# Kernel optimization log

Measured on AMD Instinct MI355X. Metric: run time of the kernel, lower is better.

The kernel has to match this reference:

```python
import jax, jax.numpy as jnp
import numpy as np

IGNORE_INDEX = -100
LABEL_SMOOTHING = 0.0


def setup_inputs() -> dict:
    key = jax.random.key(0)
    k1, k2, k3, k4 = jax.random.split(key, 4)
    BT, H, V = 4096, 1024, 32000
    x = jax.random.normal(k1, (BT, H), dtype=jnp.float32)
    target = jax.random.randint(k2, (BT,), 0, V, dtype=jnp.int64)
    # scale weight so logits have O(1) std (realistic trained lm_head scale)
    weight = jax.random.normal(k3, (V, H), dtype=jnp.float32) * 0.02
    bias = jax.random.normal(k4, (V,), dtype=jnp.float32) * 0.02
    return {"x": x, "target": target, "weight": weight, "bias": bias}


def reference(x, target, weight, bias):
    # x: [BT, H], weight: [V, H], bias: [V], target: [BT]
    V = weight.shape[0]
    ls = LABEL_SMOOTHING
    logits = x @ weight.T + bias                     # [BT, V]
    lse = jax.nn.logsumexp(logits, axis=-1)          # [BT]
    # gather logit at the target class (clip so ignore_index rows stay in-bounds)
    safe_t = jnp.clip(target, 0, V - 1)
    x_y = jnp.take_along_axis(logits, safe_t[:, None], axis=-1)[:, 0]
    # CE with label smoothing: (1-ls)*(lse - x_y) + ls*lse - (ls/V)*sum_j x_j
    per_row = (1.0 - ls) * (lse - x_y)
    if ls > 0.0:
        per_row = per_row + ls * lse - (ls / V) * jnp.sum(logits, axis=-1)
    valid = target != IGNORE_INDEX
    per_row = jnp.where(valid, per_row, 0.0)
    n_non_ignore = jnp.sum(valid).astype(per_row.dtype)
    loss = jnp.sum(per_row) / n_non_ignore
    return loss
```

## Files before the change

kernel.cpp:

```cpp
#include <hip/hip_runtime.h>
#include <hip/hip_bf16.h>
#include <stdint.h>


typedef float f16v __attribute__((ext_vector_type(16)));
typedef int v8i __attribute__((ext_vector_type(8)));
typedef int v4i __attribute__((ext_vector_type(4)));

__device__ __forceinline__ unsigned pk_fp8(float4 v) {
  int w = 0;
  w = __builtin_amdgcn_cvt_pk_fp8_f32(v.x, v.y, w, false);
  w = __builtin_amdgcn_cvt_pk_fp8_f32(v.z, v.w, w, true);
  return (unsigned)w;
}

__global__ __launch_bounds__(256) void cast_stage_k(const float* __restrict__ inW,
                                                    char* __restrict__ outW,
                                                    const float* __restrict__ inX,
                                                    char* __restrict__ outX,
                                                    int sW, int sTot) {
  __shared__ unsigned lds[8192];
  int s = blockIdx.x;
  const float* in;
  char* out;
  if (s < sW) { in = inW; out = outW; }
  else        { in = inX; out = outX; s -= sW; }
  const int t = threadIdx.x;
  const float4* src = (const float4*)in + (long)s * 8192 + t;
  const int u0 = ((t >> 3) << 8) + (t & 7);
#pragma unroll 4
  for (int r = 0; r < 32; ++r) lds[u0 + r * 8] = pk_fp8(src[r * 256]);
  __syncthreads();
  const uint4* lv = (const uint4*)lds;
  uint4* dst = (uint4*)(out + (long)s * 32768);
#pragma unroll
  for (int p = 0; p < 8; ++p) dst[p * 256 + t] = lv[p * 256 + t];
}

__device__ __forceinline__ v8i ldfrag(const char* p) {
  const v4i* q = (const v4i*)p;
  v4i lo = q[0];
  v4i hi = q[1];
  return __builtin_shufflevector(lo, hi, 0, 1, 2, 3, 4, 5, 6, 7);
}

#define MFMA1(A, B, C) \
  __builtin_amdgcn_mfma_scale_f32_32x32x64_f8f6f4(A, B, C, 0, 0, 0, 127, 0, 127)

__global__ __launch_bounds__(256, 4)
void gemm_sumexp(const char* __restrict__ Xf, const char* __restrict__ Wf,
                 const float* __restrict__ bias, float* __restrict__ partials,
                 int H, int BT) {
  __shared__ float rowsum[2][128];

  const int tid = threadIdx.x;
  const int w = tid >> 6, lane = tid & 63;
  const int wr = w >> 1, wc = w & 1;
  const int l32 = lane & 31, kh = lane >> 5;

  const int by = blockIdx.x;
  const int bx = blockIdx.y;
  const int m0 = bx * 128, n0 = by * 128;

  const int Rb = bx * 4 + wr * 2;
  const int Nb = by * 4 + wc * 2;

  const char* pA0 = Xf + (long)(Rb + 0) * 32768 + lane * 32;
  const char* pA1 = Xf + (long)(Rb + 1) * 32768 + lane * 32;
  const char* pB0 = Wf + (long)(Nb + 0) * 32768 + lane * 32;
  const char* pB1 = Wf + (long)(Nb + 1) * 32768 + lane * 32;

  f16v acc[2][2];
#pragma unroll
  for (int mi = 0; mi < 2; mi++)
#pragma unroll
    for (int ni = 0; ni < 2; ni++)
#pragma unroll
      for (int r = 0; r < 16; r++) acc[mi][ni][r] = 0.f;

  const int nG = H >> 6;
#pragma unroll 4
  for (int g = 0; g < nG; g++) {
    v8i a0 = ldfrag(pA0); pA0 += 2048;
    v8i a1 = ldfrag(pA1); pA1 += 2048;
    v8i b0 = ldfrag(pB0); pB0 += 2048;
    v8i b1 = ldfrag(pB1); pB1 += 2048;
    acc[0][0] = MFMA1(a0, b0, acc[0][0]);
    acc[0][1] = MFMA1(a0, b1, acc[0][1]);
    acc[1][0] = MFMA1(a1, b0, acc[1][0]);
    acc[1][1] = MFMA1(a1, b1, acc[1][1]);
  }

  float bv[2];
  bv[0] = bias[n0 + wc * 64 + l32];
  bv[1] = bias[n0 + wc * 64 + 32 + l32];

#pragma unroll
  for (int mi = 0; mi < 2; mi++) {
    float p[16];
#pragma unroll
    for (int r = 0; r < 16; r++) p[r] = 0.f;
#pragma unroll
    for (int ni = 0; ni < 2; ni++)
#pragma unroll
      for (int r = 0; r < 16; r++) p[r] += __expf(acc[mi][ni][r] + bv[ni]);
#pragma unroll
    for (int off = 1; off < 32; off <<= 1)
#pragma unroll
      for (int r = 0; r < 16; r++) p[r] += __shfl_xor(p[r], off, 32);
    if (l32 == 0) {
#pragma unroll
      for (int r = 0; r < 16; r++)
        rowsum[wc][wr * 64 + mi * 32 + (r & 3) + 8 * (r >> 2) + 4 * kh] = p[r];
    }
  }
  __syncthreads();
  if (tid < 128)
    partials[(long)by * BT + m0 + tid] = rowsum[0][tid] + rowsum[1][tid];
}

__global__ __launch_bounds__(256)
void row_reduce(const float* __restrict__ partials, const float* __restrict__ x,
                const float* __restrict__ wt, const float* __restrict__ bias,
                const int* __restrict__ tgt, float* __restrict__ bsum,
                float* __restrict__ bcnt, int BT, int nCB, int H, int V) {
  const int w = threadIdx.x >> 6, lane = threadIdx.x & 63;
  const int row = blockIdx.x * 4 + w;
  float S = 0.f;
  for (int b = lane; b < nCB; b += 64) S += partials[(long)b * BT + row];
  const int t = tgt[row];
  const int st = min(max(t, 0), V - 1);
  const float4* xr = (const float4*)(x + (long)row * H);
  const float4* wr = (const float4*)(wt + (long)st * H);
  float d = 0.f;
  const int n4 = H >> 2;
  for (int i = lane; i < n4; i += 64) {
    float4 a = xr[i], b = wr[i];
    d += a.x * b.x + a.y * b.y + a.z * b.z + a.w * b.w;
  }
  for (int off = 32; off; off >>= 1) {
    S += __shfl_down(S, off, 64);
    d += __shfl_down(d, off, 64);
  }
  __shared__ float sp[4], sc[4];
  if (lane == 0) {
    bool valid = (t != -100);
    sp[w] = valid ? (logf(S) - (d + bias[st])) : 0.f;
    sc[w] = valid ? 1.f : 0.f;
  }
  __syncthreads();
  if (threadIdx.x == 0) {
    bsum[blockIdx.x] = sp[0] + sp[1] + sp[2] + sp[3];
    bcnt[blockIdx.x] = sc[0] + sc[1] + sc[2] + sc[3];
  }
}

__global__ void finalize(const float* __restrict__ bsum, const float* __restrict__ bcnt,
                         float* __restrict__ out, int nb) {
  float s = 0.f, c = 0.f;
  for (int i = threadIdx.x; i < nb; i += 64) { s += bsum[i]; c += bcnt[i]; }
  for (int off = 32; off; off >>= 1) {
    s += __shfl_down(s, off, 64);
    c += __shfl_down(c, off, 64);
  }
  if (threadIdx.x == 0) out[0] = s / c;
}

extern "C" void kernel_launch(void* const* d_in, const int* in_sizes, int n_in,
                              void* d_out, int out_size, void* d_ws, size_t ws_size,
                              hipStream_t stream) {
  const float* x = (const float*)d_in[0];
  const int* tgt = (const int*)d_in[1];
  const float* w = (const float*)d_in[2];
  const float* bias = (const float*)d_in[3];
  float* out = (float*)d_out;

  const int BT = in_sizes[1];
  const int V = in_sizes[3];
  const int H = in_sizes[0] / BT;
  const int nCB = V / 128;

  char* ws = (char*)d_ws;
  const long wb_bytes = (long)V * H;
  const long xb_bytes = (long)BT * H;
  char* Wf = ws;
  char* Xf = ws + wb_bytes;
  float* partials = (float*)(ws + wb_bytes + xb_bytes);
  float* bsum = partials + (long)nCB * BT;
  float* bcnt = bsum + (BT / 4);

  const int sW = V / 32;
  const int sTot = sW + BT / 32;
  cast_stage_k<<<sTot, 256, 0, stream>>>(w, Wf, x, Xf, sW, sTot);
  dim3 grid(nCB, BT / 128);
  gemm_sumexp<<<grid, 256, 0, stream>>>(Xf, Wf, bias, partials, H, BT);
  row_reduce<<<BT / 4, 256, 0, stream>>>(partials, x, w, bias, tgt, bsum, bcnt,
                                         BT, nCB, H, V);
  finalize<<<1, 64, 0, stream>>>(bsum, bcnt, out, BT / 4);
}
```

Baseline: 398.5 us.

## Keep weight tile resident in LDS and stream all input rows per block

Each block now owns 128 vocabulary columns. It loads that fp8 weight slab (128 KB) into LDS once with global_load_lds, then loops over every 256-row slab of the fp8 input, computing MFMA tiles and writing per-slab row sums of exp. The grid shrinks to one block per column tile with 512 threads. This is meant to roughly halve global/L2 traffic by reading weights once instead of once per row tile. The trade-off is that the large LDS footprint allows only one block per CU, which lowers occupancy and latency hiding for the streamed input loads.

```diff
diff --git a/kernel.cpp b/kernel.cpp
--- a/kernel.cpp
+++ b/kernel.cpp
@@ -47,76 +47,89 @@
 #define MFMA1(A, B, C) \
   __builtin_amdgcn_mfma_scale_f32_32x32x64_f8f6f4(A, B, C, 0, 0, 0, 127, 0, 127)
 
-__global__ __launch_bounds__(256, 4)
+__global__ __launch_bounds__(512, 2)
 void gemm_sumexp(const char* __restrict__ Xf, const char* __restrict__ Wf,
                  const float* __restrict__ bias, float* __restrict__ partials,
                  int H, int BT) {
-  __shared__ float rowsum[2][128];
+  __shared__ char wlds[131072];
+  __shared__ float rowsum[2][4][256];
 
   const int tid = threadIdx.x;
   const int w = tid >> 6, lane = tid & 63;
-  const int wr = w >> 1, wc = w & 1;
+  const int wr = w >> 2, wc = w & 3;
   const int l32 = lane & 31, kh = lane >> 5;
 
   const int by = blockIdx.x;
-  const int bx = blockIdx.y;
-  const int m0 = bx * 128, n0 = by * 128;
-
-  const int Rb = bx * 4 + wr * 2;
-  const int Nb = by * 4 + wc * 2;
-
-  const char* pA0 = Xf + (long)(Rb + 0) * 32768 + lane * 32;
-  const char* pA1 = Xf + (long)(Rb + 1) * 32768 + lane * 32;
-  const char* pB0 = Wf + (long)(Nb + 0) * 32768 + lane * 32;
-  const char* pB1 = Wf + (long)(Nb + 1) * 32768 + lane * 32;
-
-  f16v acc[2][2];
-#pragma unroll
-  for (int mi = 0; mi < 2; mi++)
-#pragma unroll
-    for (int ni = 0; ni < 2; ni++)
-#pragma unroll
-      for (int r = 0; r < 16; r++) acc[mi][ni][r] = 0.f;
-
+  const int n0 = by * 128;
+
+  {
+    const char* src = Wf + (long)by * 131072 + lane * 16;
+#pragma unroll
+    for (int r = 0; r < 16; ++r) {
+      const int i = w * 16 + r;
+      __builtin_amdgcn_global_load_lds(
+          (const __attribute__((address_space(1))) void*)(src + i * 1024),
+          (__attribute__((address_space(3))) void*)(wlds + i * 1024),
+          16, 0, 0);
+    }
+  }
+  __syncthreads();
+
+  const float bv = bias[n0 + wc * 32 + l32];
   const int nG = H >> 6;
+  const int nSlab = BT >> 8;
+
+  for (int s = 0; s < nSlab; ++s) {
+    f16v acc[4];
+#pragma unroll
+    for (int mi = 0; mi < 4; mi++)
+#pragma unroll
+      for (int r = 0; r < 16; r++) acc[mi][r] = 0.f;
+
+    const int Rb = s * 8 + wr * 4;
+    const char* pA0 = Xf + (long)(Rb + 0) * 32768 + lane * 32;
+    const char* pA1 = Xf + (long)(Rb + 1) * 32768 + lane * 32;
+    const char* pA2 = Xf + (long)(Rb + 2) * 32768 + lane * 32;
+    const char* pA3 = Xf + (long)(Rb + 3) * 32768 + lane * 32;
+    const char* pB = wlds + wc * 32768 + lane * 32;
+
 #pragma unroll 4
-  for (int g = 0; g < nG; g++) {
-    v8i a0 = ldfrag(pA0); pA0 += 2048;
-    v8i a1 = ldfrag(pA1); pA1 += 2048;
-    v8i b0 = ldfrag(pB0); pB0 += 2048;
-    v8i b1 = ldfrag(pB1); pB1 += 2048;
-    acc[0][0] = MFMA1(a0, b0, acc[0][0]);
-    acc[0][1] = MFMA1(a0, b1, acc[0][1]);
-    acc[1][0] = MFMA1(a1, b0, acc[1][0]);
-    acc[1][1] = MFMA1(a1, b1, acc[1][1]);
-  }
-
-  float bv[2];
-  bv[0] = bias[n0 + wc * 64 + l32];
-  bv[1] = bias[n0 + wc * 64 + 32 + l32];
-
-#pragma unroll
-  for (int mi = 0; mi < 2; mi++) {
-    float p[16];
-#pragma unroll
-    for (int r = 0; r < 16; r++) p[r] = 0.f;
-#pragma unroll
-    for (int ni = 0; ni < 2; ni++)
-#pragma unroll
-      for (int r = 0; r < 16; r++) p[r] += __expf(acc[mi][ni][r] + bv[ni]);
-#pragma unroll
-    for (int off = 1; off < 32; off <<= 1)
-#pragma unroll
-      for (int r = 0; r < 16; r++) p[r] += __shfl_xor(p[r], off, 32);
-    if (l32 == 0) {
-#pragma unroll
-      for (int r = 0; r < 16; r++)
-        rowsum[wc][wr * 64 + mi * 32 + (r & 3) + 8 * (r >> 2) + 4 * kh] = p[r];
+    for (int g = 0; g < nG; ++g) {
+      v8i b0 = ldfrag(pB);  pB += 2048;
+      v8i a0 = ldfrag(pA0); pA0 += 2048;
+      v8i a1 = ldfrag(pA1); pA1 += 2048;
+      v8i a2 = ldfrag(pA2); pA2 += 2048;
+      v8i a3 = ldfrag(pA3); pA3 += 2048;
+      acc[0] = MFMA1(a0, b0, acc[0]);
+      acc[1] = MFMA1(a1, b0, acc[1]);
+      acc[2] = MFMA1(a2, b0, acc[2]);
+      acc[3] = MFMA1(a3, b0, acc[3]);
+      if ((g & 3) == 3) __builtin_amdgcn_s_barrier();
     }
-  }
-  __syncthreads();
-  if (tid < 128)
-    partials[(long)by * BT + m0 + tid] = rowsum[0][tid] + rowsum[1][tid];
+    pB -= (long)nG * 2048;
+
+    const int sb = s & 1;
+#pragma unroll
+    for (int mi = 0; mi < 4; mi++) {
+      float p[16];
+#pragma unroll
+      for (int r = 0; r < 16; r++) p[r] = __expf(acc[mi][r] + bv);
+#pragma unroll
+      for (int off = 1; off < 32; off <<= 1)
+#pragma unroll
+        for (int r = 0; r < 16; r++) p[r] += __shfl_xor(p[r], off, 32);
+      if (l32 == 0) {
+#pragma unroll
+        for (int r = 0; r < 16; r++)
+          rowsum[sb][wc][wr * 128 + mi * 32 + (r & 3) + 8 * (r >> 2) + 4 * kh] = p[r];
+      }
+    }
+    __syncthreads();
+    if (tid < 256)
+      partials[(long)by * BT + s * 256 + tid] =
+          rowsum[sb][0][tid] + rowsum[sb][1][tid] +
+          rowsum[sb][2][tid] + rowsum[sb][3][tid];
+  }
 }
 
 __global__ __launch_bounds__(256)
@@ -192,8 +205,7 @@
   const int sW = V / 32;
   const int sTot = sW + BT / 32;
   cast_stage_k<<<sTot, 256, 0, stream>>>(w, Wf, x, Xf, sW, sTot);
-  dim3 grid(nCB, BT / 128);
-  gemm_sumexp<<<grid, 256, 0, stream>>>(Xf, Wf, bias, partials, H, BT);
+  gemm_sumexp<<<nCB, 512, 0, stream>>>(Xf, Wf, bias, partials, H, BT);
   row_reduce<<<BT / 4, 256, 0, stream>>>(partials, x, w, bias, tgt, bsum, bcnt,
                                          BT, nCB, H, V);
   finalize<<<1, 64, 0, stream>>>(bsum, bcnt, out, BT / 4);
```

After: 477.5 us. +19.8%, slower.
